# Kernel optimization log

Measured on AMD Instinct MI355X. Metric: run time of the kernel, lower is better.

Reference implementation:

```python
import jax, jax.numpy as jnp
import numpy as np

TEMPERATURE = 8.0  # sqrt(head_dim=64)


def setup_inputs() -> dict:
    key = jax.random.key(0)
    kq, kk, kv, km = jax.random.split(key, 4)
    B, S, D = 16, 2048, 64
    q = jax.random.normal(kq, (B, S, D), dtype=jnp.float32)
    k = jax.random.normal(kk, (B, S, D), dtype=jnp.float32)
    v = jax.random.normal(kv, (B, S, D), dtype=jnp.float32)
    mask = jax.random.randint(km, (B, S, S), 0, 2).astype(jnp.bool_)
    return {"q": q, "k": k, "v": v, "mask": mask}


def reference(q, k, v, mask):
    # latent = q @ k^T / temperature  -> [B, Sq, Sk]
    latent = jnp.einsum('bqd,bkd->bqk', q, k) / TEMPERATURE
    # NOTE: the original fills masked positions with 1e-9 (NOT -inf); keep faithful.
    latent = jnp.where(mask, jnp.float32(1e-9), latent)
    attn = jax.nn.softmax(latent, axis=-1)
    return jnp.einsum('bqk,bkd->bqd', attn, v)
```

## Files before the change

kernel.cpp:

```cpp
#include <hip/hip_runtime.h>
#include <hip/hip_bf16.h>

#define BB 16
#define SS 2048
#define DD 64

typedef __attribute__((ext_vector_type(8)))  unsigned short ushort8;
typedef __attribute__((ext_vector_type(8)))  __bf16 bf16x8;
typedef __attribute__((ext_vector_type(16))) float f32x16;

static __device__ __forceinline__ unsigned short f2bf(float x) {
    return __builtin_bit_cast(unsigned short, __float2bfloat16(x));
}
static __device__ __forceinline__ unsigned pk2(float a, float b) {
    return (unsigned)f2bf(a) | ((unsigned)f2bf(b) << 16);
}

union F4 { float4 v; float a[4]; };

__global__ __launch_bounds__(256, 2)
void sdpa_mfma_kernel(const float* __restrict__ Q, const float* __restrict__ K,
                      const float* __restrict__ V, const unsigned int* __restrict__ M,
                      float* __restrict__ O) {
    __shared__ __align__(16) char smem[29184];
    char* Qs = smem;
    char* Ks = smem + 8192;
    char* Vs = smem + 16384;
    char* Ms = smem + 24576;
    float* red  = (float*)(smem + 8192);
    float* denx = (float*)(smem + 24576);

    const int t    = threadIdx.x;
    const int lane = t & 63;
    const int l31  = lane & 31;
    const int half = lane >> 5;
    const int w    = t >> 6;
    const int qs   = w & 1;
    const int kh   = w >> 1;
    const int b    = blockIdx.y;
    const int q0   = blockIdx.x * 64;

    const float* Qg = Q + ((size_t)b * SS + q0) * DD;
    const float* Kg = K + (size_t)b * SS * DD;
    const float* Vg = V + (size_t)b * SS * DD;
    const unsigned int* Mg = M + (size_t)b * SS * SS + (size_t)q0 * SS;

    const int sr = t >> 2;
    const int sc = t & 3;

    {
        F4 f0, f1, f2, f3;
        const float* src = Qg + sr * DD + sc * 16;
        f0.v = *(const float4*)(src);
        f1.v = *(const float4*)(src + 4);
        f2.v = *(const float4*)(src + 8);
        f3.v = *(const float4*)(src + 12);
        ushort8 u0, u1;
        #pragma unroll
        for (int e = 0; e < 4; e++) {
            u0[e]     = f2bf(f0.a[e] * 0.125f);
            u0[e + 4] = f2bf(f1.a[e] * 0.125f);
            u1[e]     = f2bf(f2.a[e] * 0.125f);
            u1[e + 4] = f2bf(f3.a[e] * 0.125f);
        }
        *(ushort8*)(Qs + sr * 128 + (((sc * 2)     ^ (sr & 7)) * 16)) = u0;
        *(ushort8*)(Qs + sr * 128 + (((sc * 2 + 1) ^ (sr & 7)) * 16)) = u1;
    }
    __syncthreads();

    const int qrow = 32 * qs + l31;
    ushort8 bq[4];
    #pragma unroll
    for (int dc = 0; dc < 4; dc++)
        bq[dc] = *(const ushort8*)(Qs + qrow * 128 + (((2 * dc + half) ^ (qrow & 7)) * 16));

    f32x16 On0, On1;
    #pragma unroll
    for (int i = 0; i < 16; i++) { On0[i] = 0.f; On1[i] = 0.f; }
    float den_acc = 0.f;

    const int krow = 32 * kh + l31;
    const int d0v  = (t & 15) * 4;
    const int kkb  = (t >> 4) * 2;

    for (int kt = 0; kt < SS / 64; ++kt) {
        {
            F4 f0, f1, f2, f3;
            const float* src = Kg + (size_t)(kt * 64 + sr) * DD + sc * 16;
            f0.v = *(const float4*)(src);
            f1.v = *(const float4*)(src + 4);
            f2.v = *(const float4*)(src + 8);
            f3.v = *(const float4*)(src + 12);
            ushort8 u0, u1;
            #pragma unroll
            for (int e = 0; e < 4; e++) {
                u0[e]     = f2bf(f0.a[e]);
                u0[e + 4] = f2bf(f1.a[e]);
                u1[e]     = f2bf(f2.a[e]);
                u1[e + 4] = f2bf(f3.a[e]);
            }
            *(ushort8*)(Ks + sr * 128 + (((sc * 2)     ^ (sr & 7)) * 16)) = u0;
            *(ushort8*)(Ks + sr * 128 + (((sc * 2 + 1) ^ (sr & 7)) * 16)) = u1;
        }
        {
            #pragma unroll
            for (int it2 = 0; it2 < 2; it2++) {
                const int kk = kkb + 32 * it2;
                F4 va, vb;
                va.v = *(const float4*)(Vg + (size_t)(kt * 64 + kk)     * DD + d0v);
                vb.v = *(const float4*)(Vg + (size_t)(kt * 64 + kk + 1) * DD + d0v);
                #pragma unroll
                for (int e = 0; e < 4; e++) {
                    const int d = d0v + e;
                    *(unsigned*)(Vs + d * 128 + (((kk >> 3) ^ (d & 7)) * 16) + (kk & 7) * 2)
                        = pk2(va.a[e], vb.a[e]);
                }
            }
        }
        {
            const unsigned int* Mw = Mg + (size_t)sr * SS + kt * 64 + sc * 16;
            unsigned wd[4];
            #pragma unroll
            for (int g = 0; g < 4; g++) {
                const uint4 u = *(const uint4*)(Mw + 4 * g);
                wd[g] = (u.x ? 1u : 0u) | (u.y ? 0x100u : 0u) |
                        (u.z ? 0x10000u : 0u) | (u.w ? 0x1000000u : 0u);
            }
            *(uint2*)(Ms + sr * 72 + sc * 16)     = make_uint2(wd[0], wd[1]);
            *(uint2*)(Ms + sr * 72 + sc * 16 + 8) = make_uint2(wd[2], wd[3]);
        }
        __syncthreads();

        f32x16 S;
        #pragma unroll
        for (int i = 0; i < 16; i++) S[i] = 0.f;
        #pragma unroll
        for (int dc = 0; dc < 4; dc++) {
            bf16x8 ak = __builtin_bit_cast(bf16x8,
                *(const ushort8*)(Ks + krow * 128 + (((2 * dc + half) ^ (krow & 7)) * 16)));
            S = __builtin_amdgcn_mfma_f32_32x32x16_bf16(
                    ak, __builtin_bit_cast(bf16x8, bq[dc]), S, 0, 0, 0);
        }

        float p[16];
        #pragma unroll
        for (int g = 0; g < 4; g++) {
            const unsigned mw = *(const unsigned*)(Ms + qrow * 72 + 32 * kh + 8 * g + 4 * half);
            #pragma unroll
            for (int e = 0; e < 4; e++) {
                const float ev = __expf(S[4 * g + e]);
                const float pv = ((mw >> (8 * e)) & 0xffu) ? 1.0f : ev;
                p[4 * g + e] = pv;
                den_acc += pv;
            }
        }

        #pragma unroll
        for (int s2 = 0; s2 < 2; s2++) {
            const unsigned o0 = pk2(p[8 * s2 + 0], p[8 * s2 + 1]);
            const unsigned o1 = pk2(p[8 * s2 + 2], p[8 * s2 + 3]);
            const unsigned o2 = pk2(p[8 * s2 + 4], p[8 * s2 + 5]);
            const unsigned o3 = pk2(p[8 * s2 + 6], p[8 * s2 + 7]);
            const unsigned s0 = half ? o0 : o2;
            const unsigned s1 = half ? o1 : o3;
            const unsigned r0 = (unsigned)__shfl_xor((int)s0, 32, 64);
            const unsigned r1 = (unsigned)__shfl_xor((int)s1, 32, 64);
            uint4 bu;
            bu.x = half ? r0 : o0;
            bu.y = half ? r1 : o1;
            bu.z = half ? o2 : r0;
            bu.w = half ? o3 : r1;
            const bf16x8 bp = __builtin_bit_cast(bf16x8, bu);
            #pragma unroll
            for (int dc = 0; dc < 2; dc++) {
                const int vrow = 32 * dc + l31;
                bf16x8 av = __builtin_bit_cast(bf16x8,
                    *(const ushort8*)(Vs + vrow * 128 +
                        (((4 * kh + 2 * s2 + half) ^ (vrow & 7)) * 16)));
                if (dc == 0) On0 = __builtin_amdgcn_mfma_f32_32x32x16_bf16(av, bp, On0, 0, 0, 0);
                else         On1 = __builtin_amdgcn_mfma_f32_32x32x16_bf16(av, bp, On1, 0, 0, 0);
            }
        }
        __syncthreads();
    }

    const float den_tot = den_acc + __shfl_xor(den_acc, 32, 64);

    __syncthreads();
    if (kh == 1) {
        #pragma unroll
        for (int dc = 0; dc < 2; dc++)
            #pragma unroll
            for (int g = 0; g < 4; g++) {
                const f32x16& Oc = dc ? On1 : On0;
                float4 st;
                st.x = Oc[4 * g + 0]; st.y = Oc[4 * g + 1];
                st.z = Oc[4 * g + 2]; st.w = Oc[4 * g + 3];
                *(float4*)((char*)red + qs * 8192 + (dc * 4 + g) * 1024 + lane * 16) = st;
            }
        if (lane < 32) denx[qs * 32 + l31] = den_tot;
    }
    __syncthreads();
    if (kh == 0) {
        const float inv = 1.0f / (den_tot + denx[qs * 32 + l31]);
        float* Og = O + ((size_t)b * SS + q0 + qrow) * DD;
        #pragma unroll
        for (int dc = 0; dc < 2; dc++)
            #pragma unroll
            for (int g = 0; g < 4; g++) {
                const float4 pr = *(const float4*)((char*)red + qs * 8192 + (dc * 4 + g) * 1024 + lane * 16);
                const f32x16& Oc = dc ? On1 : On0;
                float4 st;
                st.x = (Oc[4 * g + 0] + pr.x) * inv;
                st.y = (Oc[4 * g + 1] + pr.y) * inv;
                st.z = (Oc[4 * g + 2] + pr.z) * inv;
                st.w = (Oc[4 * g + 3] + pr.w) * inv;
                *(float4*)(Og + 32 * dc + 8 * g + 4 * half) = st;
            }
    }
}

extern "C" void kernel_launch(void* const* d_in, const int* in_sizes, int n_in,
                              void* d_out, int out_size, void* d_ws, size_t ws_size,
                              hipStream_t stream) {
    const float* q = (const float*)d_in[0];
    const float* k = (const float*)d_in[1];
    const float* v = (const float*)d_in[2];
    const unsigned int* m = (const unsigned int*)d_in[3];
    float* out = (float*)d_out;

    dim3 grid(SS / 64, BB);
    sdpa_mfma_kernel<<<grid, 256, 0, stream>>>(q, k, v, m, out);
}
```

Before: 473.3 us.

## Split 128-key tiles across four waves with 32-query blocks and higher occupancy

Each block now covers 32 query rows, and its four waves each take a 32-key slice of a 128-key tile. Partial outputs and denominators from three waves are reduced through shared memory at the end. The grid doubles and the launch-bounds occupancy hint rises to 4, aiming for more latency hiding on the mask stream. The trade-off is twice the K/V reloading per query and larger shared memory.

```diff
diff --git a/kernel.cpp b/kernel.cpp
--- a/kernel.cpp
+++ b/kernel.cpp
@@ -15,64 +15,53 @@
 static __device__ __forceinline__ unsigned pk2(float a, float b) {
     return (unsigned)f2bf(a) | ((unsigned)f2bf(b) << 16);
 }
-
 union F4 { float4 v; float a[4]; };
 
-__global__ __launch_bounds__(256, 2)
+__global__ __launch_bounds__(256, 4)
 void sdpa_mfma_kernel(const float* __restrict__ Q, const float* __restrict__ K,
                       const float* __restrict__ V, const unsigned int* __restrict__ M,
                       float* __restrict__ O) {
-    __shared__ __align__(16) char smem[29184];
-    char* Qs = smem;
-    char* Ks = smem + 8192;
+    __shared__ __align__(16) char smem[37120];
+    char* Ks = smem;
     char* Vs = smem + 16384;
-    char* Ms = smem + 24576;
-    float* red  = (float*)(smem + 8192);
-    float* denx = (float*)(smem + 24576);
+    char* Ms = smem + 32768;
+    char* Qs = smem + 32768;
+    float* red  = (float*)smem;
+    float* denx = (float*)(smem + 32768);
 
     const int t    = threadIdx.x;
     const int lane = t & 63;
     const int l31  = lane & 31;
     const int half = lane >> 5;
-    const int w    = t >> 6;
-    const int qs   = w & 1;
-    const int kh   = w >> 1;
+    const int kh   = t >> 6;
     const int b    = blockIdx.y;
-    const int q0   = blockIdx.x * 64;
-
-    const float* Qg = Q + ((size_t)b * SS + q0) * DD;
+    const int q0   = blockIdx.x * 32;
+
     const float* Kg = K + (size_t)b * SS * DD;
     const float* Vg = V + (size_t)b * SS * DD;
     const unsigned int* Mg = M + (size_t)b * SS * SS + (size_t)q0 * SS;
 
-    const int sr = t >> 2;
-    const int sc = t & 3;
-
     {
-        F4 f0, f1, f2, f3;
-        const float* src = Qg + sr * DD + sc * 16;
-        f0.v = *(const float4*)(src);
-        f1.v = *(const float4*)(src + 4);
-        f2.v = *(const float4*)(src + 8);
-        f3.v = *(const float4*)(src + 12);
-        ushort8 u0, u1;
+        const int sr = t >> 3, sc = t & 7;
+        const float* src = Q + ((size_t)b * SS + q0 + sr) * DD + sc * 8;
+        F4 f0, f1; f0.v = *(const float4*)src; f1.v = *(const float4*)(src + 4);
+        ushort8 u;
         #pragma unroll
         for (int e = 0; e < 4; e++) {
-            u0[e]     = f2bf(f0.a[e] * 0.125f);
-            u0[e + 4] = f2bf(f1.a[e] * 0.125f);
-            u1[e]     = f2bf(f2.a[e] * 0.125f);
-            u1[e + 4] = f2bf(f3.a[e] * 0.125f);
-        }
-        *(ushort8*)(Qs + sr * 128 + (((sc * 2)     ^ (sr & 7)) * 16)) = u0;
-        *(ushort8*)(Qs + sr * 128 + (((sc * 2 + 1) ^ (sr & 7)) * 16)) = u1;
-    }
-    __syncthreads();
-
-    const int qrow = 32 * qs + l31;
-    ushort8 bq[4];
+            u[e]     = f2bf(f0.a[e] * 0.125f);
+            u[e + 4] = f2bf(f1.a[e] * 0.125f);
+        }
+        *(ushort8*)(Qs + sr * 128 + ((sc ^ (sr & 7)) * 16)) = u;
+    }
+    __syncthreads();
+
+    const int qrow = l31;
+    bf16x8 bq[4];
     #pragma unroll
     for (int dc = 0; dc < 4; dc++)
-        bq[dc] = *(const ushort8*)(Qs + qrow * 128 + (((2 * dc + half) ^ (qrow & 7)) * 16));
+        bq[dc] = __builtin_bit_cast(bf16x8, *(const ushort8*)(
+            Qs + qrow * 128 + (((2 * dc + half) ^ (qrow & 7)) * 16)));
+    __syncthreads();
 
     f32x16 On0, On1;
     #pragma unroll
@@ -81,44 +70,40 @@
 
     const int krow = 32 * kh + l31;
     const int d0v  = (t & 15) * 4;
-    const int kkb  = (t >> 4) * 2;
-
-    for (int kt = 0; kt < SS / 64; ++kt) {
+    const int kkb  = (t >> 4) * 4;
+
+    for (int kt = 0; kt < SS / 128; ++kt) {
+        #pragma unroll
+        for (int j = 0; j < 4; j++) {
+            const int idx = 2 * t + 512 * j;
+            const int row = idx >> 4;
+            const int g   = (idx & 15) >> 1;
+            const float* src = Kg + (size_t)(kt * 128) * DD + (size_t)idx * 4;
+            F4 fa, fb; fa.v = *(const float4*)src; fb.v = *(const float4*)(src + 4);
+            ushort8 u;
+            #pragma unroll
+            for (int e = 0; e < 4; e++) { u[e] = f2bf(fa.a[e]); u[e + 4] = f2bf(fb.a[e]); }
+            *(ushort8*)(Ks + row * 128 + ((g ^ (row & 7)) * 16)) = u;
+        }
+        #pragma unroll
+        for (int it2 = 0; it2 < 2; it2++) {
+            const int kk = kkb + 64 * it2;
+            const float* src = Vg + (size_t)(kt * 128 + kk) * DD + d0v;
+            F4 r0, r1, r2, r3;
+            r0.v = *(const float4*)(src);
+            r1.v = *(const float4*)(src + DD);
+            r2.v = *(const float4*)(src + 2 * DD);
+            r3.v = *(const float4*)(src + 3 * DD);
+            #pragma unroll
+            for (int e = 0; e < 4; e++) {
+                const int d = d0v + e;
+                const uint2 wv = make_uint2(pk2(r0.a[e], r1.a[e]), pk2(r2.a[e], r3.a[e]));
+                *(uint2*)(Vs + d * 256 + (((kk >> 3) ^ (d & 15)) * 16) + (kk & 7) * 2) = wv;
+            }
+        }
         {
-            F4 f0, f1, f2, f3;
-            const float* src = Kg + (size_t)(kt * 64 + sr) * DD + sc * 16;
-            f0.v = *(const float4*)(src);
-            f1.v = *(const float4*)(src + 4);
-            f2.v = *(const float4*)(src + 8);
-            f3.v = *(const float4*)(src + 12);
-            ushort8 u0, u1;
-            #pragma unroll
-            for (int e = 0; e < 4; e++) {
-                u0[e]     = f2bf(f0.a[e]);
-                u0[e + 4] = f2bf(f1.a[e]);
-                u1[e]     = f2bf(f2.a[e]);
-                u1[e + 4] = f2bf(f3.a[e]);
-            }
-            *(ushort8*)(Ks + sr * 128 + (((sc * 2)     ^ (sr & 7)) * 16)) = u0;
-            *(ushort8*)(Ks + sr * 128 + (((sc * 2 + 1) ^ (sr & 7)) * 16)) = u1;
-        }
-        {
-            #pragma unroll
-            for (int it2 = 0; it2 < 2; it2++) {
-                const int kk = kkb + 32 * it2;
-                F4 va, vb;
-                va.v = *(const float4*)(Vg + (size_t)(kt * 64 + kk)     * DD + d0v);
-                vb.v = *(const float4*)(Vg + (size_t)(kt * 64 + kk + 1) * DD + d0v);
-                #pragma unroll
-                for (int e = 0; e < 4; e++) {
-                    const int d = d0v + e;
-                    *(unsigned*)(Vs + d * 128 + (((kk >> 3) ^ (d & 7)) * 16) + (kk & 7) * 2)
-                        = pk2(va.a[e], vb.a[e]);
-                }
-            }
-        }
-        {
-            const unsigned int* Mw = Mg + (size_t)sr * SS + kt * 64 + sc * 16;
+            const int sr = t >> 3, sc = t & 7;
+            const unsigned int* Mw = Mg + (size_t)sr * SS + kt * 128 + sc * 16;
             unsigned wd[4];
             #pragma unroll
             for (int g = 0; g < 4; g++) {
@@ -126,8 +111,8 @@
                 wd[g] = (u.x ? 1u : 0u) | (u.y ? 0x100u : 0u) |
                         (u.z ? 0x10000u : 0u) | (u.w ? 0x1000000u : 0u);
             }
-            *(uint2*)(Ms + sr * 72 + sc * 16)     = make_uint2(wd[0], wd[1]);
-            *(uint2*)(Ms + sr * 72 + sc * 16 + 8) = make_uint2(wd[2], wd[3]);
+            *(uint2*)(Ms + sr * 136 + sc * 16)     = make_uint2(wd[0], wd[1]);
+            *(uint2*)(Ms + sr * 136 + sc * 16 + 8) = make_uint2(wd[2], wd[3]);
         }
         __syncthreads();
 
@@ -136,16 +121,15 @@
         for (int i = 0; i < 16; i++) S[i] = 0.f;
         #pragma unroll
         for (int dc = 0; dc < 4; dc++) {
-            bf16x8 ak = __builtin_bit_cast(bf16x8,
-                *(const ushort8*)(Ks + krow * 128 + (((2 * dc + half) ^ (krow & 7)) * 16)));
-            S = __builtin_amdgcn_mfma_f32_32x32x16_bf16(
-                    ak, __builtin_bit_cast(bf16x8, bq[dc]), S, 0, 0, 0);
+            bf16x8 ak = __builtin_bit_cast(bf16x8, *(const ushort8*)(
+                Ks + krow * 128 + (((2 * dc + half) ^ (krow & 7)) * 16)));
+            S = __builtin_amdgcn_mfma_f32_32x32x16_bf16(ak, bq[dc], S, 0, 0, 0);
         }
 
         float p[16];
         #pragma unroll
         for (int g = 0; g < 4; g++) {
-            const unsigned mw = *(const unsigned*)(Ms + qrow * 72 + 32 * kh + 8 * g + 4 * half);
+            const unsigned mw = *(const unsigned*)(Ms + qrow * 136 + 32 * kh + 8 * g + 4 * half);
             #pragma unroll
             for (int e = 0; e < 4; e++) {
                 const float ev = __expf(S[4 * g + e]);
@@ -174,9 +158,8 @@
             #pragma unroll
             for (int dc = 0; dc < 2; dc++) {
                 const int vrow = 32 * dc + l31;
-                bf16x8 av = __builtin_bit_cast(bf16x8,
-                    *(const ushort8*)(Vs + vrow * 128 +
-                        (((4 * kh + 2 * s2 + half) ^ (vrow & 7)) * 16)));
+                bf16x8 av = __builtin_bit_cast(bf16x8, *(const ushort8*)(
+                    Vs + vrow * 256 + (((4 * kh + 2 * s2 + half) ^ (vrow & 15)) * 16)));
                 if (dc == 0) On0 = __builtin_amdgcn_mfma_f32_32x32x16_bf16(av, bp, On0, 0, 0, 0);
                 else         On1 = __builtin_amdgcn_mfma_f32_32x32x16_bf16(av, bp, On1, 0, 0, 0);
             }
@@ -187,7 +170,7 @@
     const float den_tot = den_acc + __shfl_xor(den_acc, 32, 64);
 
     __syncthreads();
-    if (kh == 1) {
+    if (kh != 0) {
         #pragma unroll
         for (int dc = 0; dc < 2; dc++)
             #pragma unroll
@@ -196,25 +179,29 @@
                 float4 st;
                 st.x = Oc[4 * g + 0]; st.y = Oc[4 * g + 1];
                 st.z = Oc[4 * g + 2]; st.w = Oc[4 * g + 3];
-                *(float4*)((char*)red + qs * 8192 + (dc * 4 + g) * 1024 + lane * 16) = st;
-            }
-        if (lane < 32) denx[qs * 32 + l31] = den_tot;
+                *(float4*)((char*)red + (kh - 1) * 8192 + (dc * 4 + g) * 1024 + lane * 16) = st;
+            }
+        if (lane < 32) denx[kh * 32 + l31] = den_tot;
     }
     __syncthreads();
     if (kh == 0) {
-        const float inv = 1.0f / (den_tot + denx[qs * 32 + l31]);
+        const float inv = 1.0f / (den_tot + denx[32 + l31] + denx[64 + l31] + denx[96 + l31]);
         float* Og = O + ((size_t)b * SS + q0 + qrow) * DD;
         #pragma unroll
         for (int dc = 0; dc < 2; dc++)
             #pragma unroll
             for (int g = 0; g < 4; g++) {
-                const float4 pr = *(const float4*)((char*)red + qs * 8192 + (dc * 4 + g) * 1024 + lane * 16);
                 const f32x16& Oc = dc ? On1 : On0;
                 float4 st;
-                st.x = (Oc[4 * g + 0] + pr.x) * inv;
-                st.y = (Oc[4 * g + 1] + pr.y) * inv;
-                st.z = (Oc[4 * g + 2] + pr.z) * inv;
-                st.w = (Oc[4 * g + 3] + pr.w) * inv;
+                st.x = Oc[4 * g + 0]; st.y = Oc[4 * g + 1];
+                st.z = Oc[4 * g + 2]; st.w = Oc[4 * g + 3];
+                #pragma unroll
+                for (int w2 = 0; w2 < 3; w2++) {
+                    const float4 pr = *(const float4*)((char*)red + w2 * 8192 +
+                                                       (dc * 4 + g) * 1024 + lane * 16);
+                    st.x += pr.x; st.y += pr.y; st.z += pr.z; st.w += pr.w;
+                }
+                st.x *= inv; st.y *= inv; st.z *= inv; st.w *= inv;
                 *(float4*)(Og + 32 * dc + 8 * g + 4 * half) = st;
             }
     }
@@ -229,6 +216,6 @@
     const unsigned int* m = (const unsigned int*)d_in[3];
     float* out = (float*)d_out;
 
-    dim3 grid(SS / 64, BB);
+    dim3 grid(SS / 32, BB);
     sdpa_mfma_kernel<<<grid, 256, 0, stream>>>(q, k, v, m, out);
 }
```

New measurement: 394.4 us. 16.7% less time.

## Prefetch next K/V/mask tile into registers and double-buffer LDS

Applied to the files above, without the earlier changes.

Global loads for the next K, V and mask tile are issued into registers before the current tile's MFMA and softmax work, then converted and written into one of two alternating LDS buffers. This hides global-load latency behind compute and removes the trailing barrier in each loop iteration. In exchange it uses more LDS per block and more registers to hold the prefetched tile, which could lower occupancy or cause spills. The V load pattern is also reshaped so each thread packs four keys per store.

```diff
diff --git a/kernel.cpp b/kernel.cpp
--- a/kernel.cpp
+++ b/kernel.cpp
@@ -4,6 +4,8 @@
 #define BB 16
 #define SS 2048
 #define DD 64
+#define NT (SS / 64)
+#define BUFS 20992
 
 typedef __attribute__((ext_vector_type(8)))  unsigned short ushort8;
 typedef __attribute__((ext_vector_type(8)))  __bf16 bf16x8;
@@ -12,23 +14,17 @@
 static __device__ __forceinline__ unsigned short f2bf(float x) {
     return __builtin_bit_cast(unsigned short, __float2bfloat16(x));
 }
-static __device__ __forceinline__ unsigned pk2(float a, float b) {
+static __device__ __forceinline__ unsigned pk2f(float a, float b) {
     return (unsigned)f2bf(a) | ((unsigned)f2bf(b) << 16);
 }
-
 union F4 { float4 v; float a[4]; };
 
 __global__ __launch_bounds__(256, 2)
 void sdpa_mfma_kernel(const float* __restrict__ Q, const float* __restrict__ K,
                       const float* __restrict__ V, const unsigned int* __restrict__ M,
                       float* __restrict__ O) {
-    __shared__ __align__(16) char smem[29184];
+    __shared__ __align__(16) char smem[8192 + 2 * BUFS];
     char* Qs = smem;
-    char* Ks = smem + 8192;
-    char* Vs = smem + 16384;
-    char* Ms = smem + 24576;
-    float* red  = (float*)(smem + 8192);
-    float* denx = (float*)(smem + 24576);
 
     const int t    = threadIdx.x;
     const int lane = t & 63;
@@ -45,12 +41,61 @@
     const float* Vg = V + (size_t)b * SS * DD;
     const unsigned int* Mg = M + (size_t)b * SS * SS + (size_t)q0 * SS;
 
-    const int sr = t >> 2;
-    const int sc = t & 3;
+    const int sr  = t >> 2;
+    const int scm = t & 3;
+    const int d0v = (t & 15) * 4;
+    const int kkv = (t >> 4) * 4;
+    const int kr0 = t >> 3;
+    const int kg0 = t & 7;
+
+    F4 ka0, ka1, ka2, ka3, va0, va1, va2, va3;
+    uint4 ma0, ma1, ma2, ma3;
+
+#define LOAD_TILE(KT) do {                                                     \
+        const float* kp_ = Kg + (size_t)(KT) * 64 * DD + 8 * t;                \
+        ka0.v = *(const float4*)(kp_);                                         \
+        ka1.v = *(const float4*)(kp_ + 4);                                     \
+        ka2.v = *(const float4*)(kp_ + 2048);                                  \
+        ka3.v = *(const float4*)(kp_ + 2052);                                  \
+        const float* vp_ = Vg + (size_t)((KT) * 64 + kkv) * DD + d0v;          \
+        va0.v = *(const float4*)(vp_);                                         \
+        va1.v = *(const float4*)(vp_ + DD);                                    \
+        va2.v = *(const float4*)(vp_ + 2 * DD);                                \
+        va3.v = *(const float4*)(vp_ + 3 * DD);                                \
+        const unsigned int* mp_ = Mg + (size_t)sr * SS + (KT) * 64 + scm * 16; \
+        ma0 = *(const uint4*)(mp_);                                            \
+        ma1 = *(const uint4*)(mp_ + 4);                                        \
+        ma2 = *(const uint4*)(mp_ + 8);                                        \
+        ma3 = *(const uint4*)(mp_ + 12);                                       \
+    } while (0)
+
+#define WRITE_TILE(Kp, Vp, Mp) do {                                            \
+        ushort8 u_;                                                            \
+        _Pragma("unroll")                                                      \
+        for (int e = 0; e < 4; e++) { u_[e] = f2bf(ka0.a[e]); u_[e+4] = f2bf(ka1.a[e]); } \
+        *(ushort8*)((Kp) + kr0 * 128 + ((kg0 ^ (kr0 & 7)) * 16)) = u_;         \
+        _Pragma("unroll")                                                      \
+        for (int e = 0; e < 4; e++) { u_[e] = f2bf(ka2.a[e]); u_[e+4] = f2bf(ka3.a[e]); } \
+        *(ushort8*)((Kp) + (kr0 + 32) * 128 + ((kg0 ^ (kr0 & 7)) * 16)) = u_;  \
+        _Pragma("unroll")                                                      \
+        for (int e = 0; e < 4; e++) {                                          \
+            const int d_ = d0v + e;                                            \
+            *(uint2*)((Vp) + d_ * 128 + (((kkv >> 3) ^ (d_ & 7)) * 16) + (kkv & 7) * 2) \
+                = make_uint2(pk2f(va0.a[e], va1.a[e]), pk2f(va2.a[e], va3.a[e])); \
+        }                                                                      \
+        const unsigned w0_ = (ma0.x?1u:0u)|(ma0.y?0x100u:0u)|(ma0.z?0x10000u:0u)|(ma0.w?0x1000000u:0u); \
+        const unsigned w1_ = (ma1.x?1u:0u)|(ma1.y?0x100u:0u)|(ma1.z?0x10000u:0u)|(ma1.w?0x1000000u:0u); \
+        const unsigned w2_ = (ma2.x?1u:0u)|(ma2.y?0x100u:0u)|(ma2.z?0x10000u:0u)|(ma2.w?0x1000000u:0u); \
+        const unsigned w3_ = (ma3.x?1u:0u)|(ma3.y?0x100u:0u)|(ma3.z?0x10000u:0u)|(ma3.w?0x1000000u:0u); \
+        *(uint2*)((Mp) + sr * 72 + scm * 16)     = make_uint2(w0_, w1_);       \
+        *(uint2*)((Mp) + sr * 72 + scm * 16 + 8) = make_uint2(w2_, w3_);       \
+    } while (0)
+
+    LOAD_TILE(0);
 
     {
         F4 f0, f1, f2, f3;
-        const float* src = Qg + sr * DD + sc * 16;
+        const float* src = Qg + sr * DD + scm * 16;
         f0.v = *(const float4*)(src);
         f1.v = *(const float4*)(src + 4);
         f2.v = *(const float4*)(src + 8);
@@ -63,8 +108,8 @@
             u1[e]     = f2bf(f2.a[e] * 0.125f);
             u1[e + 4] = f2bf(f3.a[e] * 0.125f);
         }
-        *(ushort8*)(Qs + sr * 128 + (((sc * 2)     ^ (sr & 7)) * 16)) = u0;
-        *(ushort8*)(Qs + sr * 128 + (((sc * 2 + 1) ^ (sr & 7)) * 16)) = u1;
+        *(ushort8*)(Qs + sr * 128 + (((scm * 2)     ^ (sr & 7)) * 16)) = u0;
+        *(ushort8*)(Qs + sr * 128 + (((scm * 2 + 1) ^ (sr & 7)) * 16)) = u1;
     }
     __syncthreads();
 
@@ -80,55 +125,15 @@
     float den_acc = 0.f;
 
     const int krow = 32 * kh + l31;
-    const int d0v  = (t & 15) * 4;
-    const int kkb  = (t >> 4) * 2;
-
-    for (int kt = 0; kt < SS / 64; ++kt) {
-        {
-            F4 f0, f1, f2, f3;
-            const float* src = Kg + (size_t)(kt * 64 + sr) * DD + sc * 16;
-            f0.v = *(const float4*)(src);
-            f1.v = *(const float4*)(src + 4);
-            f2.v = *(const float4*)(src + 8);
-            f3.v = *(const float4*)(src + 12);
-            ushort8 u0, u1;
-            #pragma unroll
-            for (int e = 0; e < 4; e++) {
-                u0[e]     = f2bf(f0.a[e]);
-                u0[e + 4] = f2bf(f1.a[e]);
-                u1[e]     = f2bf(f2.a[e]);
-                u1[e + 4] = f2bf(f3.a[e]);
-            }
-            *(ushort8*)(Ks + sr * 128 + (((sc * 2)     ^ (sr & 7)) * 16)) = u0;
-            *(ushort8*)(Ks + sr * 128 + (((sc * 2 + 1) ^ (sr & 7)) * 16)) = u1;
-        }
-        {
-            #pragma unroll
-            for (int it2 = 0; it2 < 2; it2++) {
-                const int kk = kkb + 32 * it2;
-                F4 va, vb;
-                va.v = *(const float4*)(Vg + (size_t)(kt * 64 + kk)     * DD + d0v);
-                vb.v = *(const float4*)(Vg + (size_t)(kt * 64 + kk + 1) * DD + d0v);
-                #pragma unroll
-                for (int e = 0; e < 4; e++) {
-                    const int d = d0v + e;
-                    *(unsigned*)(Vs + d * 128 + (((kk >> 3) ^ (d & 7)) * 16) + (kk & 7) * 2)
-                        = pk2(va.a[e], vb.a[e]);
-                }
-            }
-        }
-        {
-            const unsigned int* Mw = Mg + (size_t)sr * SS + kt * 64 + sc * 16;
-            unsigned wd[4];
-            #pragma unroll
-            for (int g = 0; g < 4; g++) {
-                const uint4 u = *(const uint4*)(Mw + 4 * g);
-                wd[g] = (u.x ? 1u : 0u) | (u.y ? 0x100u : 0u) |
-                        (u.z ? 0x10000u : 0u) | (u.w ? 0x1000000u : 0u);
-            }
-            *(uint2*)(Ms + sr * 72 + sc * 16)     = make_uint2(wd[0], wd[1]);
-            *(uint2*)(Ms + sr * 72 + sc * 16 + 8) = make_uint2(wd[2], wd[3]);
-        }
+
+    for (int kt = 0; kt < NT; ++kt) {
+        char* base = smem + 8192 + (kt & 1) * BUFS;
+        char* Kp = base;
+        char* Vp = base + 8192;
+        char* Mp = base + 16384;
+
+        WRITE_TILE(Kp, Vp, Mp);
+        if (kt + 1 < NT) LOAD_TILE(kt + 1);
         __syncthreads();
 
         f32x16 S;
@@ -137,7 +142,7 @@
         #pragma unroll
         for (int dc = 0; dc < 4; dc++) {
             bf16x8 ak = __builtin_bit_cast(bf16x8,
-                *(const ushort8*)(Ks + krow * 128 + (((2 * dc + half) ^ (krow & 7)) * 16)));
+                *(const ushort8*)(Kp + krow * 128 + (((2 * dc + half) ^ (krow & 7)) * 16)));
             S = __builtin_amdgcn_mfma_f32_32x32x16_bf16(
                     ak, __builtin_bit_cast(bf16x8, bq[dc]), S, 0, 0, 0);
         }
@@ -145,7 +150,7 @@
         float p[16];
         #pragma unroll
         for (int g = 0; g < 4; g++) {
-            const unsigned mw = *(const unsigned*)(Ms + qrow * 72 + 32 * kh + 8 * g + 4 * half);
+            const unsigned mw = *(const unsigned*)(Mp + qrow * 72 + 32 * kh + 8 * g + 4 * half);
             #pragma unroll
             for (int e = 0; e < 4; e++) {
                 const float ev = __expf(S[4 * g + e]);
@@ -157,10 +162,10 @@
 
         #pragma unroll
         for (int s2 = 0; s2 < 2; s2++) {
-            const unsigned o0 = pk2(p[8 * s2 + 0], p[8 * s2 + 1]);
-            const unsigned o1 = pk2(p[8 * s2 + 2], p[8 * s2 + 3]);
-            const unsigned o2 = pk2(p[8 * s2 + 4], p[8 * s2 + 5]);
-            const unsigned o3 = pk2(p[8 * s2 + 6], p[8 * s2 + 7]);
+            const unsigned o0 = pk2f(p[8 * s2 + 0], p[8 * s2 + 1]);
+            const unsigned o1 = pk2f(p[8 * s2 + 2], p[8 * s2 + 3]);
+            const unsigned o2 = pk2f(p[8 * s2 + 4], p[8 * s2 + 5]);
+            const unsigned o3 = pk2f(p[8 * s2 + 6], p[8 * s2 + 7]);
             const unsigned s0 = half ? o0 : o2;
             const unsigned s1 = half ? o1 : o3;
             const unsigned r0 = (unsigned)__shfl_xor((int)s0, 32, 64);
@@ -175,16 +180,17 @@
             for (int dc = 0; dc < 2; dc++) {
                 const int vrow = 32 * dc + l31;
                 bf16x8 av = __builtin_bit_cast(bf16x8,
-                    *(const ushort8*)(Vs + vrow * 128 +
+                    *(const ushort8*)(Vp + vrow * 128 +
                         (((4 * kh + 2 * s2 + half) ^ (vrow & 7)) * 16)));
                 if (dc == 0) On0 = __builtin_amdgcn_mfma_f32_32x32x16_bf16(av, bp, On0, 0, 0, 0);
                 else         On1 = __builtin_amdgcn_mfma_f32_32x32x16_bf16(av, bp, On1, 0, 0, 0);
             }
         }
-        __syncthreads();
     }
 
     const float den_tot = den_acc + __shfl_xor(den_acc, 32, 64);
+    float* red  = (float*)smem;
+    float* denx = (float*)(smem + 16384);
 
     __syncthreads();
     if (kh == 1) {
@@ -218,6 +224,8 @@
                 *(float4*)(Og + 32 * dc + 8 * g + 4 * half) = st;
             }
     }
+#undef LOAD_TILE
+#undef WRITE_TILE
 }
 
 extern "C" void kernel_launch(void* const* d_in, const int* in_sizes, int n_in,
```

Measured after the change: 394.5 us. -16.6%, faster.

## Preload full mask tile as bitmask in shared memory before key loop

Applied to the files above, without the earlier changes.

The kernel now reads the block's 64 mask rows once up front and packs them into a 16 KB shared-memory bitmask (one bit per key, rotated addressing to avoid bank conflicts), so the per-tile mask load and byte-packing stage is gone from the main loop. The V staging is reworked so each thread loads four rows and writes 8-byte packed stores, and the trailing loop barrier becomes a leading one. The aim is to take mask handling off the inner loop's critical path and cut shared-memory traffic. In exchange, the up-front pass is serial, shared-memory use grows to 40 KB (which may affect occupancy), and no mask prefetch overlaps with compute.

```diff
diff --git a/kernel.cpp b/kernel.cpp
--- a/kernel.cpp
+++ b/kernel.cpp
@@ -4,6 +4,7 @@
 #define BB 16
 #define SS 2048
 #define DD 64
+#define NT (SS / 64)
 
 typedef __attribute__((ext_vector_type(8)))  unsigned short ushort8;
 typedef __attribute__((ext_vector_type(8)))  __bf16 bf16x8;
@@ -15,20 +16,17 @@
 static __device__ __forceinline__ unsigned pk2(float a, float b) {
     return (unsigned)f2bf(a) | ((unsigned)f2bf(b) << 16);
 }
-
 union F4 { float4 v; float a[4]; };
 
 __global__ __launch_bounds__(256, 2)
 void sdpa_mfma_kernel(const float* __restrict__ Q, const float* __restrict__ K,
                       const float* __restrict__ V, const unsigned int* __restrict__ M,
                       float* __restrict__ O) {
-    __shared__ __align__(16) char smem[29184];
-    char* Qs = smem;
-    char* Ks = smem + 8192;
-    char* Vs = smem + 16384;
-    char* Ms = smem + 24576;
-    float* red  = (float*)(smem + 8192);
-    float* denx = (float*)(smem + 24576);
+    __shared__ __align__(16) char smem[40960];
+    char* Qs   = smem;
+    char* Ks   = smem + 8192;
+    char* Vs   = smem + 16384;
+    char* Bits = smem + 24576;
 
     const int t    = threadIdx.x;
     const int lane = t & 63;
@@ -43,7 +41,6 @@
     const float* Qg = Q + ((size_t)b * SS + q0) * DD;
     const float* Kg = K + (size_t)b * SS * DD;
     const float* Vg = V + (size_t)b * SS * DD;
-    const unsigned int* Mg = M + (size_t)b * SS * SS + (size_t)q0 * SS;
 
     const int sr = t >> 2;
     const int sc = t & 3;
@@ -74,6 +71,27 @@
     for (int dc = 0; dc < 4; dc++)
         bq[dc] = *(const ushort8*)(Qs + qrow * 128 + (((2 * dc + half) ^ (qrow & 7)) * 16));
 
+    {
+        const unsigned int* Mblk = M + (size_t)b * SS * SS + (size_t)q0 * SS;
+        const int kw  = t >> 2;
+        const int bsh = 8 * (t & 3);
+        for (int s = 0; s < 64; ++s) {
+            const unsigned int* rp = Mblk + (size_t)s * SS + 8 * t;
+            const uint4 a0 = *(const uint4*)(rp);
+            const uint4 a1 = *(const uint4*)(rp + 4);
+            unsigned byt = (unsigned)(a0.x != 0u)        | ((unsigned)(a0.y != 0u) << 1)
+                         | ((unsigned)(a0.z != 0u) << 2) | ((unsigned)(a0.w != 0u) << 3)
+                         | ((unsigned)(a1.x != 0u) << 4) | ((unsigned)(a1.y != 0u) << 5)
+                         | ((unsigned)(a1.z != 0u) << 6) | ((unsigned)(a1.w != 0u) << 7);
+            unsigned v = byt << bsh;
+            v |= (unsigned)__shfl_xor((int)v, 1, 64);
+            v |= (unsigned)__shfl_xor((int)v, 2, 64);
+            if ((t & 3) == 0)
+                *(unsigned*)(Bits + kw * 256 + (((s + kw) & 63) << 2)) = v;
+        }
+    }
+    __syncthreads();
+
     f32x16 On0, On1;
     #pragma unroll
     for (int i = 0; i < 16; i++) { On0[i] = 0.f; On1[i] = 0.f; }
@@ -81,9 +99,11 @@
 
     const int krow = 32 * kh + l31;
     const int d0v  = (t & 15) * 4;
-    const int kkb  = (t >> 4) * 2;
-
-    for (int kt = 0; kt < SS / 64; ++kt) {
+    const int kk4  = (t >> 4) * 4;
+
+    for (int kt = 0; kt < NT; ++kt) {
+        __syncthreads();
+
         {
             F4 f0, f1, f2, f3;
             const float* src = Kg + (size_t)(kt * 64 + sr) * DD + sc * 16;
@@ -103,31 +123,18 @@
             *(ushort8*)(Ks + sr * 128 + (((sc * 2 + 1) ^ (sr & 7)) * 16)) = u1;
         }
         {
-            #pragma unroll
-            for (int it2 = 0; it2 < 2; it2++) {
-                const int kk = kkb + 32 * it2;
-                F4 va, vb;
-                va.v = *(const float4*)(Vg + (size_t)(kt * 64 + kk)     * DD + d0v);
-                vb.v = *(const float4*)(Vg + (size_t)(kt * 64 + kk + 1) * DD + d0v);
-                #pragma unroll
-                for (int e = 0; e < 4; e++) {
-                    const int d = d0v + e;
-                    *(unsigned*)(Vs + d * 128 + (((kk >> 3) ^ (d & 7)) * 16) + (kk & 7) * 2)
-                        = pk2(va.a[e], vb.a[e]);
-                }
-            }
-        }
-        {
-            const unsigned int* Mw = Mg + (size_t)sr * SS + kt * 64 + sc * 16;
-            unsigned wd[4];
-            #pragma unroll
-            for (int g = 0; g < 4; g++) {
-                const uint4 u = *(const uint4*)(Mw + 4 * g);
-                wd[g] = (u.x ? 1u : 0u) | (u.y ? 0x100u : 0u) |
-                        (u.z ? 0x10000u : 0u) | (u.w ? 0x1000000u : 0u);
-            }
-            *(uint2*)(Ms + sr * 72 + sc * 16)     = make_uint2(wd[0], wd[1]);
-            *(uint2*)(Ms + sr * 72 + sc * 16 + 8) = make_uint2(wd[2], wd[3]);
+            const float* src = Vg + (size_t)(kt * 64 + kk4) * DD + d0v;
+            F4 r0, r1, r2, r3;
+            r0.v = *(const float4*)(src);
+            r1.v = *(const float4*)(src + DD);
+            r2.v = *(const float4*)(src + 2 * DD);
+            r3.v = *(const float4*)(src + 3 * DD);
+            #pragma unroll
+            for (int e = 0; e < 4; e++) {
+                const int d = d0v + e;
+                *(uint2*)(Vs + d * 128 + (((kk4 >> 3) ^ (d & 7)) * 16) + (kk4 & 7) * 2)
+                    = make_uint2(pk2(r0.a[e], r1.a[e]), pk2(r2.a[e], r3.a[e]));
+            }
         }
         __syncthreads();
 
@@ -142,14 +149,15 @@
                     ak, __builtin_bit_cast(bf16x8, bq[dc]), S, 0, 0, 0);
         }
 
+        const unsigned bitw = *(const unsigned*)(Bits + (2 * kt + kh) * 256 +
+                                  (((qrow + 2 * kt + kh) & 63) << 2));
         float p[16];
         #pragma unroll
         for (int g = 0; g < 4; g++) {
-            const unsigned mw = *(const unsigned*)(Ms + qrow * 72 + 32 * kh + 8 * g + 4 * half);
             #pragma unroll
             for (int e = 0; e < 4; e++) {
                 const float ev = __expf(S[4 * g + e]);
-                const float pv = ((mw >> (8 * e)) & 0xffu) ? 1.0f : ev;
+                const float pv = ((bitw >> (4 * half + 8 * g + e)) & 1u) ? 1.0f : ev;
                 p[4 * g + e] = pv;
                 den_acc += pv;
             }
@@ -181,10 +189,11 @@
                 else         On1 = __builtin_amdgcn_mfma_f32_32x32x16_bf16(av, bp, On1, 0, 0, 0);
             }
         }
-        __syncthreads();
     }
 
     const float den_tot = den_acc + __shfl_xor(den_acc, 32, 64);
+    float* red  = (float*)(smem + 8192);
+    float* denx = (float*)(smem + 24576);
 
     __syncthreads();
     if (kh == 1) {
```

New measurement: 439.5 us. 1.08x faster.
